# Kernel optimization log

Measured on AMD Instinct MI355X. Metric: run time of the kernel, lower is better.

## Reference

```python
import jax, jax.numpy as jnp
import numpy as np

N_NODES = 100000
N_EDGES = 1600000
N_GRAPHS = 1024
D_IN = 128
D_HID = 128
D_OUT = 2


def setup_inputs() -> dict:
    key = jax.random.key(0)
    ks = jax.random.split(key, 12)
    x = jax.random.normal(ks[0], (N_NODES, D_IN), dtype=jnp.float32)
    edge_index = jax.random.randint(ks[1], (2, N_EDGES), 0, N_NODES, dtype=jnp.int32)
    batch = jnp.sort(jax.random.randint(ks[2], (N_NODES,), 0, N_GRAPHS, dtype=jnp.int32))
    def lin(k, fan_in, fan_out):
        bound = 1.0 / np.sqrt(fan_in)
        kw, kb = jax.random.split(k)
        W = jax.random.uniform(kw, (fan_in, fan_out), minval=-bound, maxval=bound, dtype=jnp.float32)
        b = jax.random.uniform(kb, (fan_out,), minval=-bound, maxval=bound, dtype=jnp.float32)
        return W, b
    W1, b1 = lin(ks[3], D_IN, D_HID)
    W2, b2 = lin(ks[4], D_HID, D_HID)
    fc1_w, fc1_b = lin(ks[5], D_HID, D_HID)
    fc2_w, fc2_b = lin(ks[6], D_HID, D_OUT)
    return {"x": x, "edge_index": edge_index, "batch": batch,
            "W1": W1, "b1": b1, "W2": W2, "b2": b2,
            "fc1_w": fc1_w, "fc1_b": fc1_b, "fc2_w": fc2_w, "fc2_b": fc2_b}


def gcn_conv(x, W, b, src, dst, deg_inv_sqrt, n_nodes):
    # GCNConv: out = D^-1/2 (A + I) D^-1/2 (x W) + b, using edge list with self-loops
    h = x @ W  # [N, d_out]
    norm = deg_inv_sqrt[src] * deg_inv_sqrt[dst]  # [E+N]
    msg = h[src] * norm[:, None]  # gather + scale
    out = jnp.zeros((n_nodes, h.shape[1]), dtype=h.dtype).at[dst].add(msg)
    return out + b


def reference(x, edge_index, batch, W1, b1, W2, b2, fc1_w, fc1_b, fc2_w, fc2_b):
    n = x.shape[0]
    loops = jnp.arange(n, dtype=edge_index.dtype)
    src = jnp.concatenate([edge_index[0], loops])  # add self-loops (PyG default)
    dst = jnp.concatenate([edge_index[1], loops])
    deg = jnp.zeros((n,), dtype=x.dtype).at[dst].add(1.0)
    deg_inv_sqrt = jax.lax.rsqrt(deg)  # deg >= 1 due to self-loops

    h = jax.nn.relu(gcn_conv(x, W1, b1, src, dst, deg_inv_sqrt, n))
    # dropout p=0.5 is identity in eval mode
    h = jax.nn.relu(gcn_conv(h, W2, b2, src, dst, deg_inv_sqrt, n))

    # global_mean_pool over batch assignment
    sums = jax.ops.segment_sum(h, batch, num_segments=N_GRAPHS)
    cnts = jax.ops.segment_sum(jnp.ones((n,), dtype=h.dtype), batch, num_segments=N_GRAPHS)
    pooled = sums / jnp.maximum(cnts, 1.0)[:, None]  # [G, d]

    g = jax.nn.relu(pooled @ fc1_w + fc1_b)
    logits = g @ fc2_w + fc2_b
    return jax.nn.log_softmax(logits, axis=1)
```

## Files before the change

kernel.cpp:

```cpp
#include <hip/hip_runtime.h>
#include <hip/hip_fp16.h>
#include <math.h>


#define D_FEAT 128
#define BSHIFT 9
#define BNODES 512
#define CHUNK 4096
#define CAPB 16384
#define PCAP 16384
#define CAP 10240

using half8   = __attribute__((ext_vector_type(8))) _Float16;
using half4   = __attribute__((ext_vector_type(4))) _Float16;
using floatx4 = __attribute__((ext_vector_type(4))) float;
using floatx2 = __attribute__((ext_vector_type(2))) float;

__global__ void __launch_bounds__(256) binA_kernel(const int* __restrict__ edges,
                                                   int* __restrict__ gcur,
                                                   int* __restrict__ binned, int E, int nb) {
    __shared__ int h[256];
    __shared__ int cur[256];
    __shared__ int base[256];
    int t = threadIdx.x;
    int c0 = blockIdx.x * CHUNK;
    int sv[CHUNK / 256], bv[CHUNK / 256];
    int i0 = c0 + t * (CHUNK / 256);
    if (i0 + (CHUNK / 256) <= E) {
#pragma unroll
        for (int k = 0; k < CHUNK / 256; k += 4) {
            int4 s4 = *(const int4*)&edges[i0 + k];
            int4 d4 = *(const int4*)&edges[E + i0 + k];
            bv[k + 0] = d4.x >> BSHIFT; sv[k + 0] = ((d4.x & (BNODES - 1)) << 17) | s4.x;
            bv[k + 1] = d4.y >> BSHIFT; sv[k + 1] = ((d4.y & (BNODES - 1)) << 17) | s4.y;
            bv[k + 2] = d4.z >> BSHIFT; sv[k + 2] = ((d4.z & (BNODES - 1)) << 17) | s4.z;
            bv[k + 3] = d4.w >> BSHIFT; sv[k + 3] = ((d4.w & (BNODES - 1)) << 17) | s4.w;
        }
    } else {
#pragma unroll
        for (int k = 0; k < CHUNK / 256; ++k) {
            int i = i0 + k;
            if (i < E) {
                int s = edges[i], d = edges[E + i];
                bv[k] = d >> BSHIFT;
                sv[k] = ((d & (BNODES - 1)) << 17) | s;
            } else bv[k] = -1;
        }
    }
    h[t] = 0;
    __syncthreads();
#pragma unroll
    for (int k = 0; k < CHUNK / 256; ++k)
        if (bv[k] >= 0) atomicAdd(&h[bv[k]], 1);
    __syncthreads();
    if (t < nb && h[t] > 0) base[t] = atomicAdd(&gcur[t], h[t]);
    cur[t] = 0;
    __syncthreads();
#pragma unroll
    for (int k = 0; k < CHUNK / 256; ++k)
        if (bv[k] >= 0) {
            int b = bv[k];
            int r = atomicAdd(&cur[b], 1);
            int pos = base[b] + r;
            if (pos < CAPB) binned[b * CAPB + pos] = sv[k];
        }
}

__global__ void __launch_bounds__(256) binB_kernel(const int* __restrict__ binned,
                                                   const int* __restrict__ gcur,
                                                   float* __restrict__ dis,
                                                   int4* __restrict__ rowext,
                                                   int* __restrict__ csr,
                                                   int N, int nb) {
    __shared__ int hist[BNODES];
    __shared__ int cur[BNODES];
    __shared__ int pend[BNODES];
    __shared__ int sdata[256];
    __shared__ int vals[CAP];
    int t = threadIdx.x;
    int b = blockIdx.x;
    int node0 = b << BSHIFT;
    int cnt = gcur[b];
    const int* bin = binned + (size_t)b * CAPB;
    hist[t] = 0; hist[t + 256] = 0;
    __syncthreads();
    for (int i = t; i < cnt; i += 256) {
        int v = bin[i];
        if (i < CAP) vals[i] = v;
        atomicAdd(&hist[v >> 17], 1);
    }
    __syncthreads();
    int a0 = hist[2 * t], a1 = hist[2 * t + 1];
    int p0sz = (a0 + 15) & ~15, p1sz = (a1 + 15) & ~15;
    int pair = p0sz + p1sz;
    sdata[t] = pair;
    __syncthreads();
    for (int d = 1; d < 256; d <<= 1) {
        int u = (t >= d) ? sdata[t - d] : 0;
        __syncthreads();
        sdata[t] += u;
        __syncthreads();
    }
    int excl = sdata[t] - pair;
    int q0 = b * PCAP + excl, q1 = q0 + p0sz;
    cur[2 * t] = q0;
    cur[2 * t + 1] = q1;
    pend[2 * t] = q1;
    pend[2 * t + 1] = q1 + p1sz;
    int n0 = node0 + 2 * t, n1 = node0 + 2 * t + 1;
    if (n0 < N) {
        float d0 = rsqrtf((float)a0 + 1.0f);
        dis[n0] = d0;
        rowext[n0] = (int4){q0, q1, __float_as_int(d0), 0};
    }
    if (n1 < N) {
        float d1 = rsqrtf((float)a1 + 1.0f);
        dis[n1] = d1;
        rowext[n1] = (int4){q1, q1 + p1sz, __float_as_int(d1), 0};
    }
    __syncthreads();
    for (int i = t; i < cnt; i += 256) {
        int v = (i < CAP) ? vals[i] : bin[i];
        int p = atomicAdd(&cur[v >> 17], 1);
        csr[p] = v & 0x1FFFF;
    }
    __syncthreads();
    for (int i = t; i < BNODES; i += 256) {
        int e = pend[i];
        for (int p = cur[i]; p < e; ++p) csr[p] = N;
    }
}

__global__ void wprep_kernel(const float* __restrict__ W1, const float* __restrict__ W2,
                             _Float16* __restrict__ Wt1, _Float16* __restrict__ Wt2,
                             unsigned int* __restrict__ zrow) {
    int i = blockIdx.x * blockDim.x + threadIdx.x;
    int n = i >> 7, k = i & 127;
    Wt1[i] = (_Float16)W1[k * 128 + n];
    Wt2[i] = (_Float16)W2[k * 128 + n];
    if (i < 32) zrow[i] = 0u;
}

template <bool HALF_IN>
__global__ void __launch_bounds__(256) gemm_mfma_kernel(const void* __restrict__ Xv,
                                                        const _Float16* __restrict__ WtG,
                                                        const float* __restrict__ dis,
                                                        unsigned char* __restrict__ Y8, int N) {
    __shared__ _Float16 wt[128][136];
    int t = threadIdx.x;
    int row0 = blockIdx.x * 64;

#pragma unroll
    for (int i = 0; i < 8; ++i) {
        int c = t + i * 256;
        int r = c >> 4, c8 = (c & 15) * 8;
        *(half8*)&wt[r][c8] = *(const half8*)&WtG[r * 128 + c8];
    }

    int wave = t >> 6, lane = t & 63;
    int m = lane & 15, quad = lane >> 4;
    int grow = row0 + wave * 16 + m;

    half8 a[4];
    if (grow < N) {
        if (HALF_IN) {
            const _Float16* Xp = (const _Float16*)Xv;
#pragma unroll
            for (int k = 0; k < 4; ++k)
                a[k] = *(const half8*)&Xp[(size_t)grow * 128 + k * 32 + quad * 8];
        } else {
            const float* Xp = (const float*)Xv;
#pragma unroll
            for (int k = 0; k < 4; ++k) {
                float4 v0 = *(const float4*)&Xp[(size_t)grow * 128 + k * 32 + quad * 8];
                float4 v1 = *(const float4*)&Xp[(size_t)grow * 128 + k * 32 + quad * 8 + 4];
                a[k] = (half8){(_Float16)v0.x, (_Float16)v0.y, (_Float16)v0.z, (_Float16)v0.w,
                               (_Float16)v1.x, (_Float16)v1.y, (_Float16)v1.z, (_Float16)v1.w};
            }
        }
    } else {
#pragma unroll
        for (int k = 0; k < 4; ++k) a[k] = (half8){};
    }
    __syncthreads();

    floatx4 acc[8];
#pragma unroll
    for (int nt = 0; nt < 8; ++nt) acc[nt] = (floatx4){0.f, 0.f, 0.f, 0.f};
#pragma unroll
    for (int nt = 0; nt < 8; ++nt) {
#pragma unroll
        for (int k = 0; k < 4; ++k) {
            half8 bfr = *(const half8*)&wt[nt * 16 + m][k * 32 + quad * 8];
            acc[nt] = __builtin_amdgcn_mfma_f32_16x16x32_f16(a[k], bfr, acc[nt], 0, 0, 0);
        }
    }
    int orow = row0 + wave * 16 + quad * 4;
#pragma unroll
    for (int r = 0; r < 4; ++r) {
        int row = orow + r;
        if (row < N) {
            float dr = dis[row];
#pragma unroll
            for (int nt = 0; nt < 8; ++nt) {
                float v = acc[nt][r] * dr;
                unsigned char q =
                    (unsigned char)(__builtin_amdgcn_cvt_pk_fp8_f32(v, v, 0, false) & 0xff);
                Y8[(size_t)row * 128 + nt * 16 + m] = q;
            }
        }
    }
}

__global__ void __launch_bounds__(128) agg_kernel(const unsigned char* __restrict__ H8,
                                                  const int4* __restrict__ rowext,
                                                  const int* __restrict__ csr,
                                                  const float* __restrict__ bias,
                                                  _Float16* __restrict__ out, int N) {
    int v = (blockIdx.x * 128 + threadIdx.x) >> 6;
    int lane = threadIdx.x & 63;
    if (v >= N) return;
    int half = lane >> 5, sl = lane & 31;
    int4 re = rowext[v];
    int r0 = re.x, len = re.y - re.x;
    float dv = __int_as_float(re.z);
    unsigned fo = (unsigned)(sl << 2);

    floatx2 a01, a23;
    {
        unsigned int u = *(const unsigned int*)(H8 + (((unsigned)v << 7) | fo));
        floatx2 lo = __builtin_amdgcn_cvt_pk_f32_fp8(u, false);
        floatx2 hi = __builtin_amdgcn_cvt_pk_f32_fp8(u, true);
        floatx2 hf = {0.5f, 0.5f};
        a01 = hf * lo;
        a23 = hf * hi;
    }
    const int4* cp = (const int4*)(csr + r0);
    int4 cb0, cb1, cb2, cb3;
    if (len > 0) { cb0 = cp[0]; cb1 = cp[1]; cb2 = cp[2]; cb3 = cp[3]; }
#define ACC(uu)                                                         \
        {                                                               \
            a01 += __builtin_amdgcn_cvt_pk_f32_fp8(uu, false);          \
            a23 += __builtin_amdgcn_cvt_pk_f32_fp8(uu, true);           \
        }
    for (int base = 0; base < len; base += 16) {
        int4 c0 = cb0, c1 = cb1, c2 = cb2, c3 = cb3;
        if (base + 16 < len) {
            const int4* np = cp + ((base >> 4) + 1) * 4;
            cb0 = np[0]; cb1 = np[1]; cb2 = np[2]; cb3 = np[3];
        }
        int s0 = half ? c0.y : c0.x,  s1 = half ? c0.w : c0.z;
        int s2 = half ? c1.y : c1.x,  s3 = half ? c1.w : c1.z;
        int s4 = half ? c2.y : c2.x,  s5 = half ? c2.w : c2.z;
        int s6 = half ? c3.y : c3.x,  s7 = half ? c3.w : c3.z;
        unsigned int u0 = *(const unsigned int*)(H8 + (((unsigned)s0 << 7) | fo));
        unsigned int u1 = *(const unsigned int*)(H8 + (((unsigned)s1 << 7) | fo));
        unsigned int u2 = *(const unsigned int*)(H8 + (((unsigned)s2 << 7) | fo));
        unsigned int u3 = *(const unsigned int*)(H8 + (((unsigned)s3 << 7) | fo));
        unsigned int u4 = *(const unsigned int*)(H8 + (((unsigned)s4 << 7) | fo));
        unsigned int u5 = *(const unsigned int*)(H8 + (((unsigned)s5 << 7) | fo));
        unsigned int u6 = *(const unsigned int*)(H8 + (((unsigned)s6 << 7) | fo));
        unsigned int u7 = *(const unsigned int*)(H8 + (((unsigned)s7 << 7) | fo));
        ACC(u0) ACC(u1) ACC(u2) ACC(u3) ACC(u4) ACC(u5) ACC(u6) ACC(u7)
    }
#undef ACC
    a01[0] += __shfl_xor(a01[0], 32, 64);
    a01[1] += __shfl_xor(a01[1], 32, 64);
    a23[0] += __shfl_xor(a23[0], 32, 64);
    a23[1] += __shfl_xor(a23[1], 32, 64);
    if (half == 0) {
        float4 b = *(const float4*)&bias[sl * 4];
        half4 o = {(_Float16)fmaxf(dv * a01[0] + b.x, 0.f),
                   (_Float16)fmaxf(dv * a01[1] + b.y, 0.f),
                   (_Float16)fmaxf(dv * a23[0] + b.z, 0.f),
                   (_Float16)fmaxf(dv * a23[1] + b.w, 0.f)};
        *(half4*)&out[(size_t)v * 128 + sl * 4] = o;
    }
}

__device__ __forceinline__ int lower_bound_i(const int* a, int n, int key) {
    int lo = 0, hi = n;
    while (lo < hi) {
        int mid = (lo + hi) >> 1;
        if (a[mid] < key) lo = mid + 1;
        else hi = mid;
    }
    return lo;
}

__global__ void __launch_bounds__(512) poolhead_kernel(const _Float16* __restrict__ H,
                                                       const int* __restrict__ batch,
                                                       const float* __restrict__ fc1w,
                                                       const float* __restrict__ fc1b,
                                                       const float* __restrict__ fc2w,
                                                       const float* __restrict__ fc2b,
                                                       float* __restrict__ out, int N) {
    __shared__ int range[2];
    __shared__ float part[4][128];
    __shared__ float p[128];
    __shared__ float r0s[128], r1s[128];
    int g = blockIdx.x;
    int t = threadIdx.x;
    int j = t & 127, rg = t >> 7;
    if (t < 2) range[t] = lower_bound_i(batch, N, g + t);
    __syncthreads();
    int lo = range[0], hi = range[1];
    float s = 0.f;
    for (int v = lo + rg; v < hi; v += 4) s += (float)H[(size_t)v * 128 + j];
    part[rg][j] = s;
    __syncthreads();
    if (rg == 0) {
        float tot = part[0][j] + part[1][j] + part[2][j] + part[3][j];
        p[j] = tot / fmaxf((float)(hi - lo), 1.0f);
    }
    __syncthreads();
    if (t < 128) {
        float acc = fc1b[t];
#pragma unroll 8
        for (int k = 0; k < 128; ++k) acc = fmaf(p[k], fc1w[k * 128 + t], acc);
        float gv = fmaxf(acc, 0.f);
        r0s[t] = gv * fc2w[t * 2 + 0];
        r1s[t] = gv * fc2w[t * 2 + 1];
    }
    __syncthreads();
    for (int st = 64; st > 0; st >>= 1) {
        if (t < st) {
            r0s[t] += r0s[t + st];
            r1s[t] += r1s[t + st];
        }
        __syncthreads();
    }
    if (t == 0) {
        float l0 = r0s[0] + fc2b[0];
        float l1 = r1s[0] + fc2b[1];
        float m = fmaxf(l0, l1);
        float lse = m + logf(expf(l0 - m) + expf(l1 - m));
        out[g * 2 + 0] = l0 - lse;
        out[g * 2 + 1] = l1 - lse;
    }
}

extern "C" void kernel_launch(void* const* d_in, const int* in_sizes, int n_in,
                              void* d_out, int out_size, void* d_ws, size_t ws_size,
                              hipStream_t stream) {
    const float* x    = (const float*)d_in[0];
    const int* edges  = (const int*)d_in[1];
    const int* batch  = (const int*)d_in[2];
    const float* W1   = (const float*)d_in[3];
    const float* b1   = (const float*)d_in[4];
    const float* W2   = (const float*)d_in[5];
    const float* b2   = (const float*)d_in[6];
    const float* fc1w = (const float*)d_in[7];
    const float* fc1b = (const float*)d_in[8];
    const float* fc2w = (const float*)d_in[9];
    const float* fc2b = (const float*)d_in[10];
    float* out = (float*)d_out;

    int N = in_sizes[2];
    int E = in_sizes[1] / 2;
    int G = out_size / 2;
    int nb = (N + BNODES - 1) / BNODES;
    int nA = (E + CHUNK - 1) / CHUNK;

    char* ws = (char*)d_ws;
    size_t off = 0;
    auto alloc = [&](size_t bytes) -> char* {
        char* ptr = ws + off;
        off += (bytes + 255) & ~(size_t)255;
        return ptr;
    };
    int* gcur          = (int*)alloc((size_t)nb * 4);
    int* binned        = (int*)alloc((size_t)nb * CAPB * 4);
    int4* rowext       = (int4*)alloc((size_t)N * 16);
    float* dis         = (float*)alloc((size_t)N * 4);
    int* csr           = (int*)alloc((size_t)nb * PCAP * 4);
    _Float16* Wt1      = (_Float16*)alloc(128 * 128 * 2);
    _Float16* Wt2      = (_Float16*)alloc(128 * 128 * 2);
    unsigned char* buf8 = (unsigned char*)alloc((size_t)(N + 1) * D_FEAT);
    _Float16* bufH     = (_Float16*)alloc((size_t)N * D_FEAT * 2);

    hipMemsetAsync(gcur, 0, (size_t)nb * 4, stream);

    binA_kernel<<<nA, 256, 0, stream>>>(edges, gcur, binned, E, nb);
    binB_kernel<<<nb, 256, 0, stream>>>(binned, gcur, dis, rowext, csr, N, nb);
    wprep_kernel<<<64, 256, 0, stream>>>(W1, W2, Wt1, Wt2,
                                         (unsigned int*)(buf8 + (size_t)N * D_FEAT));

    int gAgg = (N + 1) / 2;
    int gGemm = (N + 63) / 64;
    gemm_mfma_kernel<false><<<gGemm, 256, 0, stream>>>((const void*)x, Wt1, dis, buf8, N);
    agg_kernel<<<gAgg, 128, 0, stream>>>(buf8, rowext, csr, b1, bufH, N);
    gemm_mfma_kernel<true><<<gGemm, 256, 0, stream>>>((const void*)bufH, Wt2, dis, buf8, N);
    agg_kernel<<<gAgg, 128, 0, stream>>>(buf8, rowext, csr, b2, bufH, N);
    poolhead_kernel<<<G, 512, 0, stream>>>(bufH, batch, fc1w, fc1b, fc2w, fc2b, out, N);
}
```

Baseline: 268.0 us.

## Fold weight prep into binB, widen agg blocks, unroll gather loop by 32

Merges the weight transpose/convert kernel into extra blocks of the binB kernel, removing one launch. The aggregation kernel now uses 256-thread blocks (4 nodes per block) and drops the int4 register prefetch of CSR indices. Instead it loads indices directly and processes 32 edges per iteration, with a 16-edge tail. This aims for more memory-level parallelism in the gather, at the cost of losing the explicit software prefetch of the next index chunk.

```diff
diff --git a/kernel.cpp b/kernel.cpp
--- a/kernel.cpp
+++ b/kernel.cpp
@@ -71,14 +71,27 @@
                                                    float* __restrict__ dis,
                                                    int4* __restrict__ rowext,
                                                    int* __restrict__ csr,
+                                                   const float* __restrict__ W1,
+                                                   const float* __restrict__ W2,
+                                                   _Float16* __restrict__ Wt1,
+                                                   _Float16* __restrict__ Wt2,
+                                                   unsigned int* __restrict__ zrow,
                                                    int N, int nb) {
+    int b = blockIdx.x;
+    int t = threadIdx.x;
+    if (b >= nb) {
+        int i = (b - nb) * 256 + t;
+        int n = i >> 7, k = i & 127;
+        Wt1[i] = (_Float16)W1[k * 128 + n];
+        Wt2[i] = (_Float16)W2[k * 128 + n];
+        if (i < 32) zrow[i] = 0u;
+        return;
+    }
     __shared__ int hist[BNODES];
     __shared__ int cur[BNODES];
     __shared__ int pend[BNODES];
     __shared__ int sdata[256];
     __shared__ int vals[CAP];
-    int t = threadIdx.x;
-    int b = blockIdx.x;
     int node0 = b << BSHIFT;
     int cnt = gcur[b];
     const int* bin = binned + (size_t)b * CAPB;
@@ -131,16 +144,6 @@
     }
 }
 
-__global__ void wprep_kernel(const float* __restrict__ W1, const float* __restrict__ W2,
-                             _Float16* __restrict__ Wt1, _Float16* __restrict__ Wt2,
-                             unsigned int* __restrict__ zrow) {
-    int i = blockIdx.x * blockDim.x + threadIdx.x;
-    int n = i >> 7, k = i & 127;
-    Wt1[i] = (_Float16)W1[k * 128 + n];
-    Wt2[i] = (_Float16)W2[k * 128 + n];
-    if (i < 32) zrow[i] = 0u;
-}
-
 template <bool HALF_IN>
 __global__ void __launch_bounds__(256) gemm_mfma_kernel(const void* __restrict__ Xv,
                                                         const _Float16* __restrict__ WtG,
@@ -212,12 +215,12 @@
     }
 }
 
-__global__ void __launch_bounds__(128) agg_kernel(const unsigned char* __restrict__ H8,
+__global__ void __launch_bounds__(256) agg_kernel(const unsigned char* __restrict__ H8,
                                                   const int4* __restrict__ rowext,
                                                   const int* __restrict__ csr,
                                                   const float* __restrict__ bias,
                                                   _Float16* __restrict__ out, int N) {
-    int v = (blockIdx.x * 128 + threadIdx.x) >> 6;
+    int v = (blockIdx.x * blockDim.x + threadIdx.x) >> 6;
     int lane = threadIdx.x & 63;
     if (v >= N) return;
     int half = lane >> 5, sl = lane & 31;
@@ -235,34 +238,35 @@
         a01 = hf * lo;
         a23 = hf * hi;
     }
-    const int4* cp = (const int4*)(csr + r0);
-    int4 cb0, cb1, cb2, cb3;
-    if (len > 0) { cb0 = cp[0]; cb1 = cp[1]; cb2 = cp[2]; cb3 = cp[3]; }
 #define ACC(uu)                                                         \
         {                                                               \
             a01 += __builtin_amdgcn_cvt_pk_f32_fp8(uu, false);          \
             a23 += __builtin_amdgcn_cvt_pk_f32_fp8(uu, true);           \
         }
-    for (int base = 0; base < len; base += 16) {
-        int4 c0 = cb0, c1 = cb1, c2 = cb2, c3 = cb3;
-        if (base + 16 < len) {
-            const int4* np = cp + ((base >> 4) + 1) * 4;
-            cb0 = np[0]; cb1 = np[1]; cb2 = np[2]; cb3 = np[3];
-        }
-        int s0 = half ? c0.y : c0.x,  s1 = half ? c0.w : c0.z;
-        int s2 = half ? c1.y : c1.x,  s3 = half ? c1.w : c1.z;
-        int s4 = half ? c2.y : c2.x,  s5 = half ? c2.w : c2.z;
-        int s6 = half ? c3.y : c3.x,  s7 = half ? c3.w : c3.z;
-        unsigned int u0 = *(const unsigned int*)(H8 + (((unsigned)s0 << 7) | fo));
-        unsigned int u1 = *(const unsigned int*)(H8 + (((unsigned)s1 << 7) | fo));
-        unsigned int u2 = *(const unsigned int*)(H8 + (((unsigned)s2 << 7) | fo));
-        unsigned int u3 = *(const unsigned int*)(H8 + (((unsigned)s3 << 7) | fo));
-        unsigned int u4 = *(const unsigned int*)(H8 + (((unsigned)s4 << 7) | fo));
-        unsigned int u5 = *(const unsigned int*)(H8 + (((unsigned)s5 << 7) | fo));
-        unsigned int u6 = *(const unsigned int*)(H8 + (((unsigned)s6 << 7) | fo));
-        unsigned int u7 = *(const unsigned int*)(H8 + (((unsigned)s7 << 7) | fo));
+#define GATHER(ss) *(const unsigned int*)(H8 + (((unsigned)(ss) << 7) | fo))
+    int base = 0;
+    for (; base + 32 <= len; base += 32) {
+        int e = r0 + base + half;
+        int s0 = csr[e],      s1 = csr[e + 2],  s2 = csr[e + 4],  s3 = csr[e + 6];
+        int s4 = csr[e + 8],  s5 = csr[e + 10], s6 = csr[e + 12], s7 = csr[e + 14];
+        int s8 = csr[e + 16], s9 = csr[e + 18], sa = csr[e + 20], sb = csr[e + 22];
+        int sc = csr[e + 24], sd = csr[e + 26], se = csr[e + 28], sf = csr[e + 30];
+        unsigned int u0 = GATHER(s0), u1 = GATHER(s1), u2 = GATHER(s2), u3 = GATHER(s3);
+        unsigned int u4 = GATHER(s4), u5 = GATHER(s5), u6 = GATHER(s6), u7 = GATHER(s7);
+        unsigned int u8 = GATHER(s8), u9 = GATHER(s9), ua = GATHER(sa), ub = GATHER(sb);
+        unsigned int uc = GATHER(sc), ud = GATHER(sd), ue = GATHER(se), uf = GATHER(sf);
         ACC(u0) ACC(u1) ACC(u2) ACC(u3) ACC(u4) ACC(u5) ACC(u6) ACC(u7)
-    }
+        ACC(u8) ACC(u9) ACC(ua) ACC(ub) ACC(uc) ACC(ud) ACC(ue) ACC(uf)
+    }
+    if (base + 16 <= len) {
+        int e = r0 + base + half;
+        int s0 = csr[e],      s1 = csr[e + 2],  s2 = csr[e + 4],  s3 = csr[e + 6];
+        int s4 = csr[e + 8],  s5 = csr[e + 10], s6 = csr[e + 12], s7 = csr[e + 14];
+        unsigned int u0 = GATHER(s0), u1 = GATHER(s1), u2 = GATHER(s2), u3 = GATHER(s3);
+        unsigned int u4 = GATHER(s4), u5 = GATHER(s5), u6 = GATHER(s6), u7 = GATHER(s7);
+        ACC(u0) ACC(u1) ACC(u2) ACC(u3) ACC(u4) ACC(u5) ACC(u6) ACC(u7)
+    }
+#undef GATHER
 #undef ACC
     a01[0] += __shfl_xor(a01[0], 32, 64);
     a01[1] += __shfl_xor(a01[1], 32, 64);
@@ -382,15 +386,16 @@
     hipMemsetAsync(gcur, 0, (size_t)nb * 4, stream);
 
     binA_kernel<<<nA, 256, 0, stream>>>(edges, gcur, binned, E, nb);
-    binB_kernel<<<nb, 256, 0, stream>>>(binned, gcur, dis, rowext, csr, N, nb);
-    wprep_kernel<<<64, 256, 0, stream>>>(W1, W2, Wt1, Wt2,
-                                         (unsigned int*)(buf8 + (size_t)N * D_FEAT));
-
-    int gAgg = (N + 1) / 2;
+    binB_kernel<<<nb + 64, 256, 0, stream>>>(binned, gcur, dis, rowext, csr,
+                                             W1, W2, Wt1, Wt2,
+                                             (unsigned int*)(buf8 + (size_t)N * D_FEAT),
+                                             N, nb);
+
+    int gAgg = (N * 64 + 255) / 256;
     int gGemm = (N + 63) / 64;
     gemm_mfma_kernel<false><<<gGemm, 256, 0, stream>>>((const void*)x, Wt1, dis, buf8, N);
-    agg_kernel<<<gAgg, 128, 0, stream>>>(buf8, rowext, csr, b1, bufH, N);
+    agg_kernel<<<gAgg, 256, 0, stream>>>(buf8, rowext, csr, b1, bufH, N);
     gemm_mfma_kernel<true><<<gGemm, 256, 0, stream>>>((const void*)bufH, Wt2, dis, buf8, N);
-    agg_kernel<<<gAgg, 128, 0, stream>>>(buf8, rowext, csr, b2, bufH, N);
+    agg_kernel<<<gAgg, 256, 0, stream>>>(buf8, rowext, csr, b2, bufH, N);
     poolhead_kernel<<<G, 512, 0, stream>>>(bufH, batch, fc1w, fc1b, fc2w, fc2b, out, N);
 }
```

New measurement: 257.7 us. 3.9% less time.
